# Performance work log

Hardware: AMD Instinct MI355X
Metric: run time of the kernel (lower is better)

## Reference

```python
import jax, jax.numpy as jnp
import numpy as np

B, D, C = 512, 256, 200000
S_SCALE = 30.0
MARGIN = 0.2
EPS_NORM = 1e-12  # torch F.normalize default eps


def setup_inputs() -> dict:
    key = jax.random.key(0)
    k1, k2, k3 = jax.random.split(key, 3)
    inputs = jax.random.normal(k1, (B, D, 1), dtype=jnp.float32)
    # module inits weight ~ N(0, 0.01)
    weight = 0.01 * jax.random.normal(k2, (C, D, 1), dtype=jnp.float32)
    targets = jax.random.randint(k3, (B,), 0, C, dtype=jnp.int64)
    return {"inputs": inputs, "weight": weight, "targets": targets}


def _l2norm(x, axis):
    n = jnp.sqrt(jnp.sum(x * x, axis=axis, keepdims=True))
    return x / jnp.maximum(n, EPS_NORM)


def reference(inputs, weight, targets):
    x = inputs[:, :, 0]            # [B, D]
    w = weight[:, :, 0]            # [C, D]
    xn = _l2norm(x, axis=1)
    wn = _l2norm(w, axis=1)
    cosine = jnp.einsum('bd,cd->bc', xn, wn)          # [B, C]
    rows = jnp.arange(B)
    cos_t = cosine[rows, targets]                     # [B]
    penalty = cos_t - MARGIN                          # AM margin, lambda_factor=0
    logits = S_SCALE * cosine.at[rows, targets].set(penalty)  # [B, C]
    # CrossEntropyLoss(reduction='mean') on logits / t with t=1
    lse = jax.nn.logsumexp(logits, axis=1)            # [B]
    nll = lse - logits[rows, targets]
    return jnp.mean(nll)
```

## Files before the change

kernel.cpp:

```cpp
#include <hip/hip_runtime.h>
#include <hip/hip_bf16.h>
#include <stdint.h>

#define BDIM 512
#define CDIM 200000
#define DDIM 256
#define S_SC 30.0f
#define MARG 0.2f

#define BN 128
#define NBLK 1563
#define NBLK_PAD 1568

typedef float f4 __attribute__((ext_vector_type(4)));
typedef float f32x4 __attribute__((ext_vector_type(4)));
typedef short bf16x8 __attribute__((ext_vector_type(8)));
typedef unsigned short u16x4 __attribute__((ext_vector_type(4)));

__device__ __forceinline__ unsigned short f2bf(float f) {
  unsigned int u = __float_as_uint(f);
  u += 0x7FFF + ((u >> 16) & 1);
  return (unsigned short)(u >> 16);
}

__device__ __forceinline__ float wave_allsum(float v) {
#pragma unroll
  for (int off = 32; off >= 1; off >>= 1) v += __shfl_xor(v, off);
  return v;
}

__global__ __launch_bounds__(512) void k_xfrag(const float* __restrict__ x,
                                               unsigned short* __restrict__ xn_frag) {
  __shared__ float xtile[16][260];
  __shared__ float sscale[16];
  const int tid = threadIdx.x;
  const int lane = tid & 63;
  const int wv = tid >> 6;
  const int bt = blockIdx.x;

  #pragma unroll
  for (int h = 0; h < 2; ++h) {
    const int r = wv * 2 + h;
    f4 v = *(const f4*)(x + (size_t)(bt * 16 + r) * DDIM + lane * 4);
    float ssq = v[0]*v[0] + v[1]*v[1] + v[2]*v[2] + v[3]*v[3];
    ssq = wave_allsum(ssq);
    if (lane == 0) sscale[r] = 1.0f / fmaxf(sqrtf(ssq), 1e-12f);
    *(f4*)&xtile[r][lane * 4] = v;
  }
  __syncthreads();

  const int kk = wv;
  const int r = lane & 15;
  const int c0f = kk * 32 + (lane >> 4) * 8;
  const float sc = sscale[r];
  f4 a = *(const f4*)&xtile[r][c0f];
  f4 b = *(const f4*)&xtile[r][c0f + 4];
  bf16x8 o;
  o[0] = (short)f2bf(a[0]*sc); o[1] = (short)f2bf(a[1]*sc);
  o[2] = (short)f2bf(a[2]*sc); o[3] = (short)f2bf(a[3]*sc);
  o[4] = (short)f2bf(b[0]*sc); o[5] = (short)f2bf(b[1]*sc);
  o[6] = (short)f2bf(b[2]*sc); o[7] = (short)f2bf(b[3]*sc);
  *(bf16x8*)(xn_frag + ((size_t)(bt * 8 + kk) * 64 + lane) * 8) = o;
}

__global__ __launch_bounds__(512, 4) void k_gemm(const float* __restrict__ w,
                                                 const unsigned short* __restrict__ xn_frag,
                                                 float* __restrict__ partial_t) {
  __shared__ char wb[BN * 512];
  const int tid = threadIdx.x;
  const int lane = tid & 63;
  const int wv = tid >> 6;
  const int c0 = blockIdx.x * BN;

  f4 v[16];
  #pragma unroll
  for (int rr = 0; rr < 16; ++rr) {
    const int cg = c0 + wv * 16 + rr;
    f4 z = {0.f, 0.f, 0.f, 0.f};
    v[rr] = (cg < CDIM) ? *(const f4*)(w + (size_t)cg * DDIM + lane * 4) : z;
  }
  float ss[16];
  #pragma unroll
  for (int rr = 0; rr < 16; ++rr)
    ss[rr] = v[rr][0]*v[rr][0] + v[rr][1]*v[rr][1] + v[rr][2]*v[rr][2] + v[rr][3]*v[rr][3];
  #pragma unroll
  for (int off = 32; off >= 1; off >>= 1) {
    #pragma unroll
    for (int rr = 0; rr < 16; ++rr) ss[rr] += __shfl_xor(ss[rr], off);
  }
  #pragma unroll
  for (int rr = 0; rr < 16; ++rr) {
    const int row = wv * 16 + rr;
    const float sc = 1.0f / fmaxf(sqrtf(ss[rr]), 1e-12f);
    u16x4 o;
    o[0] = f2bf(v[rr][0]*sc); o[1] = f2bf(v[rr][1]*sc);
    o[2] = f2bf(v[rr][2]*sc); o[3] = f2bf(v[rr][3]*sc);
    const int byte = (row * 512 + lane * 8) ^ ((row & 7) << 4);
    *(u16x4*)(wb + byte) = o;
  }
  __syncthreads();

  #pragma unroll 1
  for (int o2 = 0; o2 < 2; ++o2) {
    bf16x8 bf[2][8];
    #pragma unroll
    for (int bt2 = 0; bt2 < 2; ++bt2) {
      const int bt = wv * 4 + o2 * 2 + bt2;
      #pragma unroll
      for (int kkk = 0; kkk < 8; ++kkk)
        bf[bt2][kkk] = *(const bf16x8*)(xn_frag + ((size_t)(bt * 8 + kkk) * 64 + lane) * 8);
    }
    float e0 = 0.f, e1 = 0.f;
    #pragma unroll 1
    for (int cf = 0; cf < 8; ++cf) {
      bf16x8 af[8];
      const int arow = cf * 16 + (lane & 15);
      const int asw = (arow & 7) << 4;
      #pragma unroll
      for (int kkk = 0; kkk < 8; ++kkk) {
        const int byte = (arow * 512 + kkk * 64 + (lane >> 4) * 16) ^ asw;
        af[kkk] = *(const bf16x8*)(wb + byte);
      }
      f32x4 a0 = {0.f,0.f,0.f,0.f}, a1 = {0.f,0.f,0.f,0.f};
      #pragma unroll
      for (int kkk = 0; kkk < 8; ++kkk) {
        a0 = __builtin_amdgcn_mfma_f32_16x16x32_bf16(af[kkk], bf[0][kkk], a0, 0, 0, 0);
        a1 = __builtin_amdgcn_mfma_f32_16x16x32_bf16(af[kkk], bf[1][kkk], a1, 0, 0, 0);
      }
      #pragma unroll
      for (int q = 0; q < 4; ++q) {
        const int cls = c0 + cf * 16 + (lane >> 4) * 4 + q;
        const bool ok = (cls < CDIM);
        e0 += ok ? __expf(S_SC * a0[q]) : 0.f;
        e1 += ok ? __expf(S_SC * a1[q]) : 0.f;
      }
    }
    e0 += __shfl_xor(e0, 16); e0 += __shfl_xor(e0, 32);
    e1 += __shfl_xor(e1, 16); e1 += __shfl_xor(e1, 32);
    const int bt0 = wv * 4 + o2 * 2;
    if (lane < 16) {
      partial_t[(size_t)(bt0 * 16 + lane) * NBLK_PAD + blockIdx.x] = e0;
      partial_t[(size_t)((bt0 + 1) * 16 + lane) * NBLK_PAD + blockIdx.x] = e1;
    }
  }
}

__global__ __launch_bounds__(256) void k_row(const float* __restrict__ partial_t,
                                             const float* __restrict__ x,
                                             const float* __restrict__ w,
                                             const int* __restrict__ tg,
                                             float* __restrict__ nll) {
  const int b = blockIdx.x;
  const int tid = threadIdx.x;
  const int lane = tid & 63;
  const int wv = tid >> 6;
  __shared__ float s4[4];
  __shared__ float sct;

  const float* p = partial_t + (size_t)b * NBLK_PAD;
  float s = 0.f;
  for (int r = tid; r < NBLK; r += 256) s += p[r];
  s = wave_allsum(s);
  if (lane == 0) s4[wv] = s;

  if (wv == 0) {
    const int t = tg[b];
    f4 xv = *(const f4*)(x + (size_t)b * DDIM + lane * 4);
    f4 wv4 = *(const f4*)(w + (size_t)t * DDIM + lane * 4);
    float sx = xv[0]*xv[0] + xv[1]*xv[1] + xv[2]*xv[2] + xv[3]*xv[3];
    float sw = wv4[0]*wv4[0] + wv4[1]*wv4[1] + wv4[2]*wv4[2] + wv4[3]*wv4[3];
    float sd = xv[0]*wv4[0] + xv[1]*wv4[1] + xv[2]*wv4[2] + xv[3]*wv4[3];
    sx = wave_allsum(sx);
    sw = wave_allsum(sw);
    sd = wave_allsum(sd);
    if (lane == 0)
      sct = sd / (fmaxf(sqrtf(sx), 1e-12f) * fmaxf(sqrtf(sw), 1e-12f));
  }
  __syncthreads();

  if (tid == 0) {
    const float sumexp = s4[0] + s4[1] + s4[2] + s4[3];
    const float ct = sct;
    const float tl = S_SC * (ct - MARG);
    const float adj = sumexp - __expf(S_SC * ct) + __expf(tl);
    nll[b] = logf(adj) - tl;
  }
}

__global__ __launch_bounds__(512) void k_final(const float* __restrict__ nll,
                                               float* __restrict__ out) {
  const int tid = threadIdx.x;
  float v = nll[tid];
  v = wave_allsum(v);
  __shared__ float s8[8];
  if ((tid & 63) == 0) s8[tid >> 6] = v;
  __syncthreads();
  if (tid == 0) {
    float t = 0.f;
    #pragma unroll
    for (int i = 0; i < 8; ++i) t += s8[i];
    out[0] = t / (float)BDIM;
  }
}

extern "C" void kernel_launch(void* const* d_in, const int* in_sizes, int n_in,
                              void* d_out, int out_size, void* d_ws, size_t ws_size,
                              hipStream_t stream) {
  const float* x = (const float*)d_in[0];
  const float* w = (const float*)d_in[1];
  const int* tg = (const int*)d_in[2];

  char* ws = (char*)d_ws;
  unsigned short* xn_frag = (unsigned short*)ws;
  float* partial_t = (float*)(ws + 262144);
  float* nll = (float*)(ws + 262144 + (size_t)BDIM * NBLK_PAD * 4);

  k_xfrag<<<32, 512, 0, stream>>>(x, xn_frag);
  k_gemm<<<NBLK, 512, 0, stream>>>(w, xn_frag, partial_t);
  k_row<<<BDIM, 256, 0, stream>>>(partial_t, x, w, tg, nll);
  k_final<<<1, 512, 0, stream>>>(nll, (float*)d_out);
}
```

Before: 332.6 us.

## Drop class bounds mask, transpose partial sums layout, unroll exp loop

The padded classes in the last block now skip the bounds check. Their zero weight rows give cosine 0 and exp 1, so a constant 64 is subtracted from each row's sum afterwards. The partial-sum buffer changes from row-major [B][block] to [block][B], so each GEMM block writes contiguously, and the reduction kernel now reads with a stride. The exp becomes exp2f with a prescaled constant, the class-fragment loop is fully unrolled, and the occupancy hint drops from 4 to 3 blocks per CU. Register pressure rises and the row-reduction reads become strided in exchange.

Result: slower. 616.9 us (+85.5%).

```diff
diff --git a/kernel.cpp b/kernel.cpp
--- a/kernel.cpp
+++ b/kernel.cpp
@@ -7,10 +7,11 @@
 #define DDIM 256
 #define S_SC 30.0f
 #define MARG 0.2f
+#define LOG2E_S 43.2808512f
 
 #define BN 128
 #define NBLK 1563
-#define NBLK_PAD 1568
+#define NPAD 64.0f
 
 typedef float f4 __attribute__((ext_vector_type(4)));
 typedef float f32x4 __attribute__((ext_vector_type(4)));
@@ -63,9 +64,9 @@
   *(bf16x8*)(xn_frag + ((size_t)(bt * 8 + kk) * 64 + lane) * 8) = o;
 }
 
-__global__ __launch_bounds__(512, 4) void k_gemm(const float* __restrict__ w,
+__global__ __launch_bounds__(512, 3) void k_gemm(const float* __restrict__ w,
                                                  const unsigned short* __restrict__ xn_frag,
-                                                 float* __restrict__ partial_t) {
+                                                 float* __restrict__ partial) {
   __shared__ char wb[BN * 512];
   const int tid = threadIdx.x;
   const int lane = tid & 63;
@@ -111,7 +112,7 @@
         bf[bt2][kkk] = *(const bf16x8*)(xn_frag + ((size_t)(bt * 8 + kkk) * 64 + lane) * 8);
     }
     float e0 = 0.f, e1 = 0.f;
-    #pragma unroll 1
+    #pragma unroll
     for (int cf = 0; cf < 8; ++cf) {
       bf16x8 af[8];
       const int arow = cf * 16 + (lane & 15);
@@ -129,23 +130,21 @@
       }
       #pragma unroll
       for (int q = 0; q < 4; ++q) {
-        const int cls = c0 + cf * 16 + (lane >> 4) * 4 + q;
-        const bool ok = (cls < CDIM);
-        e0 += ok ? __expf(S_SC * a0[q]) : 0.f;
-        e1 += ok ? __expf(S_SC * a1[q]) : 0.f;
+        e0 += exp2f(a0[q] * LOG2E_S);
+        e1 += exp2f(a1[q] * LOG2E_S);
       }
     }
     e0 += __shfl_xor(e0, 16); e0 += __shfl_xor(e0, 32);
     e1 += __shfl_xor(e1, 16); e1 += __shfl_xor(e1, 32);
     const int bt0 = wv * 4 + o2 * 2;
     if (lane < 16) {
-      partial_t[(size_t)(bt0 * 16 + lane) * NBLK_PAD + blockIdx.x] = e0;
-      partial_t[(size_t)((bt0 + 1) * 16 + lane) * NBLK_PAD + blockIdx.x] = e1;
+      partial[(size_t)blockIdx.x * BDIM + bt0 * 16 + lane] = e0;
+      partial[(size_t)blockIdx.x * BDIM + (bt0 + 1) * 16 + lane] = e1;
     }
   }
 }
 
-__global__ __launch_bounds__(256) void k_row(const float* __restrict__ partial_t,
+__global__ __launch_bounds__(256) void k_row(const float* __restrict__ partial,
                                              const float* __restrict__ x,
                                              const float* __restrict__ w,
                                              const int* __restrict__ tg,
@@ -157,9 +156,8 @@
   __shared__ float s4[4];
   __shared__ float sct;
 
-  const float* p = partial_t + (size_t)b * NBLK_PAD;
   float s = 0.f;
-  for (int r = tid; r < NBLK; r += 256) s += p[r];
+  for (int r = tid; r < NBLK; r += 256) s += partial[(size_t)r * BDIM + b];
   s = wave_allsum(s);
   if (lane == 0) s4[wv] = s;
 
@@ -179,7 +177,7 @@
   __syncthreads();
 
   if (tid == 0) {
-    const float sumexp = s4[0] + s4[1] + s4[2] + s4[3];
+    const float sumexp = s4[0] + s4[1] + s4[2] + s4[3] - NPAD;
     const float ct = sct;
     const float tl = S_SC * (ct - MARG);
     const float adj = sumexp - __expf(S_SC * ct) + __expf(tl);
@@ -212,11 +210,11 @@
 
   char* ws = (char*)d_ws;
   unsigned short* xn_frag = (unsigned short*)ws;
-  float* partial_t = (float*)(ws + 262144);
-  float* nll = (float*)(ws + 262144 + (size_t)BDIM * NBLK_PAD * 4);
+  float* partial = (float*)(ws + 262144);
+  float* nll = (float*)(ws + 262144 + (size_t)NBLK * BDIM * 4);
 
   k_xfrag<<<32, 512, 0, stream>>>(x, xn_frag);
-  k_gemm<<<NBLK, 512, 0, stream>>>(w, xn_frag, partial_t);
-  k_row<<<BDIM, 256, 0, stream>>>(partial_t, x, w, tg, nll);
+  k_gemm<<<NBLK, 512, 0, stream>>>(w, xn_frag, partial);
+  k_row<<<BDIM, 256, 0, stream>>>(partial, x, w, tg, nll);
   k_final<<<1, 512, 0, stream>>>(nll, (float*)d_out);
 }
```
